# Kernel optimization log

Hardware: AMD Instinct MI355X
Metric: run time of the kernel (lower is better)

## Reference

```python
import jax, jax.numpy as jnp
import numpy as np

N = 50000
E = 800000
IN_DIM = 256
HID = 128
OUT = 64


def setup_inputs() -> dict:
    key = jax.random.key(0)
    ks = jax.random.split(key, 12)
    inp = {}
    inp["x"] = jax.random.normal(ks[0], (N, IN_DIM), dtype=jnp.float32)
    inp["edge_index"] = jax.random.randint(ks[1], (2, E), 0, N, dtype=jnp.int64)
    s0 = 1.0 / np.sqrt(IN_DIM)
    inp["W0"] = jax.random.uniform(ks[2], (IN_DIM, HID), jnp.float32, -s0, s0)
    inp["b0"] = jax.random.uniform(ks[3], (HID,), jnp.float32, -s0, s0)
    sa = 1.0 / np.sqrt(2 * HID)
    inp["att_w1"] = jax.random.uniform(ks[4], (2 * HID, 1), jnp.float32, -sa, sa)
    inp["att_b1"] = jax.random.uniform(ks[5], (1,), jnp.float32, -sa, sa)
    inp["eps1"] = jnp.float32(0.1)
    inp["att_w2"] = jax.random.uniform(ks[6], (2 * HID, 1), jnp.float32, -sa, sa)
    inp["att_b2"] = jax.random.uniform(ks[7], (1,), jnp.float32, -sa, sa)
    inp["eps2"] = jnp.float32(0.1)
    sc = 1.0 / np.sqrt(HID)
    inp["Wc"] = jax.random.uniform(ks[8], (HID, OUT), jnp.float32, -sc, sc)
    inp["bc"] = jax.random.uniform(ks[9], (OUT,), jnp.float32, -sc, sc)
    return inp


def _fagcn_layer(x, row, col, att_w, att_b, eps):
    # x: [N, H]; row/col: [E]
    x_i = x[row]                       # [E, H] source (gathered)
    x_j = x[col]                       # [E, H] destination
    # cat([x_i, x_j]) @ att_w == x_i @ att_w[:H] + x_j @ att_w[H:]
    H = x.shape[1]
    score = x_i @ att_w[:H] + x_j @ att_w[H:] + att_b  # [E, 1]
    alpha = jnp.tanh(score)            # [E, 1]
    messages = alpha * x_i             # [E, H]
    agg = jax.ops.segment_sum(messages, col, num_segments=x.shape[0])  # [N, H]
    return eps * x + (1.0 - eps) * agg


def reference(x, edge_index, W0, b0, att_w1, att_b1, eps1, att_w2, att_b2, eps2, Wc, bc):
    row, col = edge_index[0], edge_index[1]
    h = jax.nn.relu(x @ W0 + b0)       # initial linear + relu (dropout=eval identity)
    h = jax.nn.relu(_fagcn_layer(h, row, col, att_w1, att_b1, eps1))
    h = jax.nn.relu(_fagcn_layer(h, row, col, att_w2, att_b2, eps2))
    return h @ Wc + bc                 # [N, OUT]
```

## Files before the change

### kernel.cpp

```cpp
#include <hip/hip_runtime.h>

#define N_NODES 50000
#define E_EDGES 800000
#define IN_DIM 256
#define HID 128
#define OUT_DIM 64
#define SLOT 64
#define RSLOT 16

#define LR 64
#define KS 64
#define KP 72
#define HP 136

#define NBUILD ((E_EDGES / 8 + 255) / 256)
#define NLIN ((N_NODES + LR - 1) / LR)


typedef unsigned short u16;
typedef __attribute__((ext_vector_type(8))) short short8;
typedef __attribute__((ext_vector_type(4))) float floatx4;

__device__ __forceinline__ u16 f2bf(float f) {
    unsigned u = __float_as_uint(f);
    unsigned r = (u + 0x7FFFu + ((u >> 16) & 1u)) >> 16;
    return (u16)r;
}
__device__ __forceinline__ void bf8_unpack(uint4 v, float* f) {
    f[0] = __uint_as_float(v.x << 16); f[1] = __uint_as_float(v.x & 0xffff0000u);
    f[2] = __uint_as_float(v.y << 16); f[3] = __uint_as_float(v.y & 0xffff0000u);
    f[4] = __uint_as_float(v.z << 16); f[5] = __uint_as_float(v.z & 0xffff0000u);
    f[6] = __uint_as_float(v.w << 16); f[7] = __uint_as_float(v.w & 0xffff0000u);
}
__device__ __forceinline__ uint4 bf8_pack(const float* f) {
    uint4 o;
    o.x = f2bf(f[0]) | ((unsigned)f2bf(f[1]) << 16);
    o.y = f2bf(f[2]) | ((unsigned)f2bf(f[3]) << 16);
    o.z = f2bf(f[4]) | ((unsigned)f2bf(f[5]) << 16);
    o.w = f2bf(f[6]) | ((unsigned)f2bf(f[7]) << 16);
    return o;
}

__global__ __launch_bounds__(256) void k_pre(const float* __restrict__ W0,
                                             const float* __restrict__ Wc,
                                             u16* __restrict__ W0T,
                                             u16* __restrict__ Wct,
                                             int* __restrict__ cnt8) {
    const int gid = blockIdx.x * 256 + threadIdx.x;
    for (int i = gid; i < 8 * N_NODES / 4; i += 32768)
        ((int4*)cnt8)[i] = (int4){0, 0, 0, 0};
    if (gid < IN_DIM * HID) {
        const int n = gid >> 8, k = gid & (IN_DIM - 1);
        W0T[gid] = f2bf(W0[k * HID + n]);
    }
    if (gid < HID * OUT_DIM) {
        const int o = gid >> 7, k = gid & (HID - 1);
        Wct[gid] = f2bf(Wc[k * OUT_DIM + o]);
    }
}

__global__ __launch_bounds__(256) void k_front(
    const float* __restrict__ x, const u16* __restrict__ W0T,
    const float* __restrict__ b0, const float* __restrict__ aw1,
    u16* __restrict__ h, float* __restrict__ sa, float* __restrict__ sb,
    const int* __restrict__ ei, int* __restrict__ cnt8,
    u16* __restrict__ srcidx2) {
    __shared__ u16 As[LR][KP];
    __shared__ u16 Bs[HID][KP];

    if (blockIdx.x < NBUILD) {
        int xcd;
        asm volatile("s_getreg_b32 %0, hwreg(HW_REG_XCC_ID, 0, 32)" : "=s"(xcd));
        xcd &= 7;
        const int cbase = xcd * N_NODES;
        const int rbase = xcd * (N_NODES * RSLOT);
        const int gid = blockIdx.x * 256 + threadIdx.x;
        if (gid >= E_EDGES / 8) return;
        const int4 w0 = ((const int4*)ei)[2 * gid];
        const int4 w1 = ((const int4*)ei)[2 * gid + 1];
        const int4 c0 = ((const int4*)(ei + E_EDGES))[2 * gid];
        const int4 c1 = ((const int4*)(ei + E_EDGES))[2 * gid + 1];
        #define AADD(c) __hip_atomic_fetch_add(&cnt8[cbase + (c)], 1, \
                        __ATOMIC_RELAXED, __HIP_MEMORY_SCOPE_WORKGROUP)
        const int p0 = AADD(c0.x);
        const int p1 = AADD(c0.y);
        const int p2 = AADD(c0.z);
        const int p3 = AADD(c0.w);
        const int p4 = AADD(c1.x);
        const int p5 = AADD(c1.y);
        const int p6 = AADD(c1.z);
        const int p7 = AADD(c1.w);
        #undef AADD
        if (p0 < RSLOT) srcidx2[rbase + (c0.x << 4) + p0] = (u16)w0.x;
        if (p1 < RSLOT) srcidx2[rbase + (c0.y << 4) + p1] = (u16)w0.y;
        if (p2 < RSLOT) srcidx2[rbase + (c0.z << 4) + p2] = (u16)w0.z;
        if (p3 < RSLOT) srcidx2[rbase + (c0.w << 4) + p3] = (u16)w0.w;
        if (p4 < RSLOT) srcidx2[rbase + (c1.x << 4) + p4] = (u16)w1.x;
        if (p5 < RSLOT) srcidx2[rbase + (c1.y << 4) + p5] = (u16)w1.y;
        if (p6 < RSLOT) srcidx2[rbase + (c1.z << 4) + p6] = (u16)w1.z;
        if (p7 < RSLOT) srcidx2[rbase + (c1.w << 4) + p7] = (u16)w1.w;
        return;
    }

    const int t = threadIdx.x;
    const int lane = t & 63;
    const int w = t >> 6;
    const int sub = lane & 15;
    const int quad = lane >> 4;
    const int row0 = (blockIdx.x - NBUILD) * LR;

    floatx4 acc[8];
    #pragma unroll
    for (int i = 0; i < 8; ++i) acc[i] = (floatx4){0.f, 0.f, 0.f, 0.f};

    const int ar = t >> 2;
    const int ak = (t & 3) * 16;
    const int sr = t >> 1;
    const int sk = (t & 1) * 32;

    for (int k0 = 0; k0 < IN_DIM; k0 += KS) {
        {
            int gr = row0 + ar;
            if (gr > N_NODES - 1) gr = N_NODES - 1;
            const float* src = x + (size_t)gr * IN_DIM + k0 + ak;
            #pragma unroll
            for (int i = 0; i < 2; ++i) {
                float4 f0 = ((const float4*)src)[2 * i];
                float4 f1 = ((const float4*)src)[2 * i + 1];
                uint4 p;
                p.x = f2bf(f0.x) | ((unsigned)f2bf(f0.y) << 16);
                p.y = f2bf(f0.z) | ((unsigned)f2bf(f0.w) << 16);
                p.z = f2bf(f1.x) | ((unsigned)f2bf(f1.y) << 16);
                p.w = f2bf(f1.z) | ((unsigned)f2bf(f1.w) << 16);
                *(uint4*)&As[ar][ak + 8 * i] = p;
            }
            const u16* wsrc = W0T + (size_t)sr * IN_DIM + k0 + sk;
            #pragma unroll
            for (int i = 0; i < 4; ++i)
                *(uint4*)&Bs[sr][sk + 8 * i] = ((const uint4*)wsrc)[i];
        }
        __syncthreads();
        #pragma unroll
        for (int kk = 0; kk < KS; kk += 32) {
            short8 a0 = *(const short8*)&As[w * 16 + sub][kk + quad * 8];
            #pragma unroll
            for (int ct = 0; ct < 8; ++ct) {
                short8 bb = *(const short8*)&Bs[ct * 16 + sub][kk + quad * 8];
                acc[ct] = __builtin_amdgcn_mfma_f32_16x16x32_bf16(a0, bb, acc[ct], 0, 0, 0);
            }
        }
        __syncthreads();
    }

    float bias[8], w1c[8], w2c[8];
    #pragma unroll
    for (int ct = 0; ct < 8; ++ct) {
        const int col = ct * 16 + sub;
        bias[ct] = b0[col];
        w1c[ct] = aw1[col];
        w2c[ct] = aw1[HID + col];
    }
    #pragma unroll
    for (int reg = 0; reg < 4; ++reg) {
        const int gr = row0 + w * 16 + quad * 4 + reg;
        const bool ok = gr < N_NODES;
        float ps = 0.f, pd = 0.f;
        #pragma unroll
        for (int ct = 0; ct < 8; ++ct) {
            const float val = fmaxf(acc[ct][reg] + bias[ct], 0.f);
            if (ok) h[(size_t)gr * HID + ct * 16 + sub] = f2bf(val);
            ps += val * w1c[ct];
            pd += val * w2c[ct];
        }
        #pragma unroll
        for (int off = 1; off < 16; off <<= 1) {
            ps += __shfl_xor(ps, off);
            pd += __shfl_xor(pd, off);
        }
        if (sub == 0 && ok) { sa[gr] = ps; sb[gr] = pd; }
    }
}

template <bool REG>
__global__ __launch_bounds__(256) void k_agg(const u16* __restrict__ hin,
                                             const float* __restrict__ sa,
                                             const float* __restrict__ sb,
                                             const float* __restrict__ attb,
                                             const float* __restrict__ epsp,
                                             const int* __restrict__ cnt_or_deg,
                                             const u16* __restrict__ srcin,
                                             u16* __restrict__ hout,
                                             const float* __restrict__ attw_next,
                                             float* __restrict__ sa_next,
                                             float* __restrict__ sb_next,
                                             u16* __restrict__ srcout,
                                             int* __restrict__ degout) {
    __shared__ u16 elist[REG ? 16 : 1][SLOT];
    const int qid = threadIdx.x >> 4;
    const int sub = threadIdx.x & 15;
    const int n = blockIdx.x * 16 + qid;
    if (n >= N_NODES) return;
    const float b = attb[0];
    const float sbn = sb[n];

    int deg;
    if constexpr (REG) {
        int c = 0;
        if (sub < 8) {
            c = cnt_or_deg[sub * N_NODES + n];
            if (c > RSLOT) c = RSLOT;
        }
        int scan = c;
        #pragma unroll
        for (int d = 1; d < 8; d <<= 1) {
            const int tv = __shfl_up(scan, d, 16);
            if (sub >= d) scan += tv;
        }
        const int off = scan - c;
        int D = __shfl(scan, 7, 16);
        if (D > SLOT) D = SLOT;
        if (sub < 8 && c > 0) {
            const u16* s2 = srcin + (size_t)sub * (N_NODES * RSLOT) + ((size_t)n << 4);
            const uint4 i0 = *(const uint4*)s2;
            const uint4 i1 = *(const uint4*)(s2 + 8);
            const unsigned dw[8] = {i0.x, i0.y, i0.z, i0.w, i1.x, i1.y, i1.z, i1.w};
            #pragma unroll
            for (int j = 0; j < 16; ++j) {
                const u16 val = (u16)(dw[j >> 1] >> ((j & 1) * 16));
                const int dp = off + j;
                if (j < c && dp < SLOT) elist[qid][dp] = val;
            }
        }
        deg = D;
        if (sub < 8 && sub * 8 < deg)
            *(uint4*)(srcout + ((size_t)n << 6) + sub * 8) =
                *(const uint4*)&elist[qid][sub * 8];
        if (sub == 0) degout[n] = deg;
    } else {
        deg = cnt_or_deg[n];
        if (deg > SLOT) deg = SLOT;
    }

    float acc[8];
    #pragma unroll
    for (int j = 0; j < 8; ++j) acc[j] = 0.f;

    const u16* dlist = REG ? nullptr : srcin + ((size_t)n << 6);
    int le = 0;
    uint4 svn;
    if constexpr (!REG) { if (le + 8 <= deg) svn = *(const uint4*)(dlist); }
    for (; le + 8 <= deg; le += 8) {
        uint4 sv;
        if constexpr (REG) {
            sv = *(const uint4*)&elist[qid][le];
        } else {
            sv = svn;
            if (le + 16 <= deg) svn = *(const uint4*)(dlist + le + 8);
        }
        int s[8];
        s[0] = (int)(sv.x & 0xffffu); s[1] = (int)(sv.x >> 16);
        s[2] = (int)(sv.y & 0xffffu); s[3] = (int)(sv.y >> 16);
        s[4] = (int)(sv.z & 0xffffu); s[5] = (int)(sv.z >> 16);
        s[6] = (int)(sv.w & 0xffffu); s[7] = (int)(sv.w >> 16);
        uint4 v[8];
        #pragma unroll
        for (int i = 0; i < 8; ++i)
            v[i] = *(const uint4*)(hin + (size_t)s[i] * HID + sub * 8);
        const float tt = tanhf(sa[s[sub & 7]] + sbn + b);
        float al[8];
        #pragma unroll
        for (int i = 0; i < 8; ++i) al[i] = __shfl(tt, i, 16);
        #pragma unroll
        for (int i = 0; i < 8; ++i) {
            float f[8];
            bf8_unpack(v[i], f);
            #pragma unroll
            for (int j = 0; j < 8; ++j) acc[j] += al[i] * f[j];
        }
    }
    const int rem = deg - le;
    if (rem > 0) {
        int s[8];
        if constexpr (REG) {
            const uint4 sv = *(const uint4*)&elist[qid][le];
            int sr8[8];
            sr8[0] = (int)(sv.x & 0xffffu); sr8[1] = (int)(sv.x >> 16);
            sr8[2] = (int)(sv.y & 0xffffu); sr8[3] = (int)(sv.y >> 16);
            sr8[4] = (int)(sv.z & 0xffffu); sr8[5] = (int)(sv.z >> 16);
            sr8[6] = (int)(sv.w & 0xffffu); sr8[7] = (int)(sv.w >> 16);
            #pragma unroll
            for (int i = 0; i < 8; ++i) s[i] = (i < rem) ? sr8[i] : sr8[0];
        } else {
            const int sfirst = (int)dlist[le];
            #pragma unroll
            for (int i = 0; i < 8; ++i) s[i] = (i < rem) ? (int)dlist[le + i] : sfirst;
        }
        const float tt = ((sub & 7) < rem) ? tanhf(sa[s[sub & 7]] + sbn + b) : 0.f;
        float al[8];
        #pragma unroll
        for (int i = 0; i < 8; ++i) al[i] = __shfl(tt, i, 16);
        #pragma unroll
        for (int i = 0; i < 8; ++i) {
            if (i < rem) {
                const uint4 v = *(const uint4*)(hin + (size_t)s[i] * HID + sub * 8);
                float f[8];
                bf8_unpack(v, f);
                #pragma unroll
                for (int j = 0; j < 8; ++j) acc[j] += al[i] * f[j];
            }
        }
    }

    const float eps = epsp[0];
    const float om = 1.f - eps;
    const uint4 sv = *(const uint4*)(hin + (size_t)n * HID + sub * 8);
    float self[8], hv[8];
    bf8_unpack(sv, self);
    #pragma unroll
    for (int j = 0; j < 8; ++j)
        hv[j] = fmaxf(eps * self[j] + om * acc[j], 0.f);
    *(uint4*)(hout + (size_t)n * HID + sub * 8) = bf8_pack(hv);

    if (attw_next != nullptr) {
        float psum = 0.f, dsum = 0.f;
        #pragma unroll
        for (int j = 0; j < 8; ++j) {
            psum += hv[j] * attw_next[sub * 8 + j];
            dsum += hv[j] * attw_next[HID + sub * 8 + j];
        }
        #pragma unroll
        for (int off = 1; off < 16; off <<= 1) {
            psum += __shfl_xor(psum, off);
            dsum += __shfl_xor(dsum, off);
        }
        if (sub == 0) { sa_next[n] = psum; sb_next[n] = dsum; }
    }
}

__global__ __launch_bounds__(256) void k_out_mfma(const u16* __restrict__ h,
                                                  const u16* __restrict__ Wct,
                                                  const float* __restrict__ bc,
                                                  float* __restrict__ out) {
    __shared__ u16 Hs[LR][HP];
    const int t = threadIdx.x;
    const int lane = t & 63;
    const int w = t >> 6;
    const int sub = lane & 15;
    const int quad = lane >> 4;
    const int row0 = blockIdx.x * LR;

    {
        const int hr = t >> 2;
        const int hc = (t & 3) * 32;
        int gr = row0 + hr;
        if (gr > N_NODES - 1) gr = N_NODES - 1;
        const u16* src = h + (size_t)gr * HID + hc;
        #pragma unroll
        for (int i = 0; i < 4; ++i)
            *(uint4*)&Hs[hr][hc + 8 * i] = ((const uint4*)src)[i];
    }
    __syncthreads();

    floatx4 acc[4];
    #pragma unroll
    for (int j = 0; j < 4; ++j) acc[j] = (floatx4){0.f, 0.f, 0.f, 0.f};

    #pragma unroll
    for (int ks = 0; ks < 4; ++ks) {
        const int ko = ks * 32 + quad * 8;
        short8 a = *(const short8*)&Hs[w * 16 + sub][ko];
        #pragma unroll
        for (int ct = 0; ct < 4; ++ct) {
            short8 bb = *(const short8*)(Wct + (ct * 16 + sub) * HID + ko);
            acc[ct] = __builtin_amdgcn_mfma_f32_16x16x32_bf16(a, bb, acc[ct], 0, 0, 0);
        }
    }

    #pragma unroll
    for (int ct = 0; ct < 4; ++ct) {
        const float bias = bc[ct * 16 + sub];
        #pragma unroll
        for (int reg = 0; reg < 4; ++reg) {
            const int gr = row0 + w * 16 + quad * 4 + reg;
            if (gr < N_NODES)
                out[(size_t)gr * OUT_DIM + ct * 16 + sub] = acc[ct][reg] + bias;
        }
    }
}

extern "C" void kernel_launch(void* const* d_in, const int* in_sizes, int n_in,
                              void* d_out, int out_size, void* d_ws, size_t ws_size,
                              hipStream_t stream) {
    const float* x   = (const float*)d_in[0];
    const int*   ei  = (const int*)d_in[1];
    const float* W0  = (const float*)d_in[2];
    const float* b0  = (const float*)d_in[3];
    const float* aw1 = (const float*)d_in[4];
    const float* ab1 = (const float*)d_in[5];
    const float* e1  = (const float*)d_in[6];
    const float* aw2 = (const float*)d_in[7];
    const float* ab2 = (const float*)d_in[8];
    const float* e2  = (const float*)d_in[9];
    const float* Wc  = (const float*)d_in[10];
    const float* bc  = (const float*)d_in[11];
    float* out = (float*)d_out;

    u16* hA  = (u16*)d_ws;
    u16* hB  = hA + (size_t)N_NODES * HID;
    u16* W0T = hB + (size_t)N_NODES * HID;
    u16* Wct = W0T + IN_DIM * HID;
    float* sa1 = (float*)(Wct + HID * OUT_DIM);
    float* sb1 = sa1 + N_NODES;
    float* sa2 = sb1 + N_NODES;
    float* sb2 = sa2 + N_NODES;
    int* deg    = (int*)(sb2 + N_NODES);
    u16* srcidx = (u16*)(deg + N_NODES);
    int* cnt8   = (int*)(srcidx + (size_t)N_NODES * SLOT);
    u16* srcidx2 = (u16*)d_out;

    k_pre<<<128, 256, 0, stream>>>(W0, Wc, W0T, Wct, cnt8);
    k_front<<<NBUILD + NLIN, 256, 0, stream>>>(x, W0T, b0, aw1, hA, sa1, sb1,
                                               ei, cnt8, srcidx2);
    k_agg<true><<<(N_NODES + 15) / 16, 256, 0, stream>>>(
        hA, sa1, sb1, ab1, e1, cnt8, srcidx2, hB, aw2, sa2, sb2, srcidx, deg);
    k_agg<false><<<(N_NODES + 15) / 16, 256, 0, stream>>>(
        hB, sa2, sb2, ab2, e2, deg, srcidx, hA, nullptr, nullptr, nullptr,
        nullptr, nullptr);
    k_out_mfma<<<NLIN, 256, 0, stream>>>(hA, Wct, bc, out);
}
```

Before: 234.0 us.

## Prefetch full x row slice into registers and batch more edges per build thread

The linear front path now loads all four K-slices of the thread's x row into registers up front and converts them to bf16 before the MFMA loop. This takes global-load latency out of the per-slice sync loop, at the cost of much higher register pressure. The edge-bucketing path now gives each thread 16 edges, up from 8, which cuts the number of build blocks. That raises per-thread atomic work but lowers launch and scheduling overhead.

```diff
diff --git a/kernel.cpp b/kernel.cpp
--- a/kernel.cpp
+++ b/kernel.cpp
@@ -13,7 +13,8 @@
 #define KP 72
 #define HP 136
 
-#define NBUILD ((E_EDGES / 8 + 255) / 256)
+#define EPT 16
+#define NBUILD ((E_EDGES + 256 * EPT - 1) / (256 * EPT))
 #define NLIN ((N_NODES + LR - 1) / LR)
 
 
@@ -73,32 +74,27 @@
         asm volatile("s_getreg_b32 %0, hwreg(HW_REG_XCC_ID, 0, 32)" : "=s"(xcd));
         xcd &= 7;
         const int cbase = xcd * N_NODES;
-        const int rbase = xcd * (N_NODES * RSLOT);
-        const int gid = blockIdx.x * 256 + threadIdx.x;
-        if (gid >= E_EDGES / 8) return;
-        const int4 w0 = ((const int4*)ei)[2 * gid];
-        const int4 w1 = ((const int4*)ei)[2 * gid + 1];
-        const int4 c0 = ((const int4*)(ei + E_EDGES))[2 * gid];
-        const int4 c1 = ((const int4*)(ei + E_EDGES))[2 * gid + 1];
-        #define AADD(c) __hip_atomic_fetch_add(&cnt8[cbase + (c)], 1, \
-                        __ATOMIC_RELAXED, __HIP_MEMORY_SCOPE_WORKGROUP)
-        const int p0 = AADD(c0.x);
-        const int p1 = AADD(c0.y);
-        const int p2 = AADD(c0.z);
-        const int p3 = AADD(c0.w);
-        const int p4 = AADD(c1.x);
-        const int p5 = AADD(c1.y);
-        const int p6 = AADD(c1.z);
-        const int p7 = AADD(c1.w);
-        #undef AADD
-        if (p0 < RSLOT) srcidx2[rbase + (c0.x << 4) + p0] = (u16)w0.x;
-        if (p1 < RSLOT) srcidx2[rbase + (c0.y << 4) + p1] = (u16)w0.y;
-        if (p2 < RSLOT) srcidx2[rbase + (c0.z << 4) + p2] = (u16)w0.z;
-        if (p3 < RSLOT) srcidx2[rbase + (c0.w << 4) + p3] = (u16)w0.w;
-        if (p4 < RSLOT) srcidx2[rbase + (c1.x << 4) + p4] = (u16)w1.x;
-        if (p5 < RSLOT) srcidx2[rbase + (c1.y << 4) + p5] = (u16)w1.y;
-        if (p6 < RSLOT) srcidx2[rbase + (c1.z << 4) + p6] = (u16)w1.z;
-        if (p7 < RSLOT) srcidx2[rbase + (c1.w << 4) + p7] = (u16)w1.w;
+        const int rb = xcd * (N_NODES * RSLOT);
+        const int base = (blockIdx.x * 256 + threadIdx.x) * EPT;
+        #pragma unroll
+        for (int g = 0; g < EPT / 4; ++g) {
+            const int eb = base + g * 4;
+            if (eb < E_EDGES) {
+                const int4 w = ((const int4*)ei)[eb >> 2];
+                const int4 c = ((const int4*)(ei + E_EDGES))[eb >> 2];
+                #define AADD(cc) __hip_atomic_fetch_add(&cnt8[cbase + (cc)], 1, \
+                                __ATOMIC_RELAXED, __HIP_MEMORY_SCOPE_WORKGROUP)
+                const int q0 = AADD(c.x);
+                const int q1 = AADD(c.y);
+                const int q2 = AADD(c.z);
+                const int q3 = AADD(c.w);
+                #undef AADD
+                if (q0 < RSLOT) srcidx2[rb + (c.x << 4) + q0] = (u16)w.x;
+                if (q1 < RSLOT) srcidx2[rb + (c.y << 4) + q1] = (u16)w.y;
+                if (q2 < RSLOT) srcidx2[rb + (c.z << 4) + q2] = (u16)w.z;
+                if (q3 < RSLOT) srcidx2[rb + (c.w << 4) + q3] = (u16)w.w;
+            }
+        }
         return;
     }
 
@@ -109,36 +105,48 @@
     const int quad = lane >> 4;
     const int row0 = (blockIdx.x - NBUILD) * LR;
 
-    floatx4 acc[8];
-    #pragma unroll
-    for (int i = 0; i < 8; ++i) acc[i] = (floatx4){0.f, 0.f, 0.f, 0.f};
-
     const int ar = t >> 2;
     const int ak = (t & 3) * 16;
     const int sr = t >> 1;
     const int sk = (t & 1) * 32;
 
-    for (int k0 = 0; k0 < IN_DIM; k0 += KS) {
-        {
-            int gr = row0 + ar;
-            if (gr > N_NODES - 1) gr = N_NODES - 1;
-            const float* src = x + (size_t)gr * IN_DIM + k0 + ak;
-            #pragma unroll
-            for (int i = 0; i < 2; ++i) {
-                float4 f0 = ((const float4*)src)[2 * i];
-                float4 f1 = ((const float4*)src)[2 * i + 1];
-                uint4 p;
-                p.x = f2bf(f0.x) | ((unsigned)f2bf(f0.y) << 16);
-                p.y = f2bf(f0.z) | ((unsigned)f2bf(f0.w) << 16);
-                p.z = f2bf(f1.x) | ((unsigned)f2bf(f1.y) << 16);
-                p.w = f2bf(f1.z) | ((unsigned)f2bf(f1.w) << 16);
-                *(uint4*)&As[ar][ak + 8 * i] = p;
-            }
-            const u16* wsrc = W0T + (size_t)sr * IN_DIM + k0 + sk;
-            #pragma unroll
-            for (int i = 0; i < 4; ++i)
-                *(uint4*)&Bs[sr][sk + 8 * i] = ((const uint4*)wsrc)[i];
-        }
+    int gr_a = row0 + ar;
+    if (gr_a > N_NODES - 1) gr_a = N_NODES - 1;
+    const float* xsrc = x + (size_t)gr_a * IN_DIM + ak;
+    float4 xr[4][4];
+    #pragma unroll
+    for (int s = 0; s < 4; ++s)
+        #pragma unroll
+        for (int i = 0; i < 4; ++i)
+            xr[s][i] = ((const float4*)(xsrc + s * KS))[i];
+    uint4 xa[4][2];
+    #pragma unroll
+    for (int s = 0; s < 4; ++s)
+        #pragma unroll
+        for (int i = 0; i < 2; ++i) {
+            const float4 f0 = xr[s][2 * i];
+            const float4 f1 = xr[s][2 * i + 1];
+            uint4 pk;
+            pk.x = f2bf(f0.x) | ((unsigned)f2bf(f0.y) << 16);
+            pk.y = f2bf(f0.z) | ((unsigned)f2bf(f0.w) << 16);
+            pk.z = f2bf(f1.x) | ((unsigned)f2bf(f1.y) << 16);
+            pk.w = f2bf(f1.z) | ((unsigned)f2bf(f1.w) << 16);
+            xa[s][i] = pk;
+        }
+
+    floatx4 acc[8];
+    #pragma unroll
+    for (int i = 0; i < 8; ++i) acc[i] = (floatx4){0.f, 0.f, 0.f, 0.f};
+
+    #pragma unroll
+    for (int s = 0; s < 4; ++s) {
+        const int k0 = s * KS;
+        *(uint4*)&As[ar][ak] = xa[s][0];
+        *(uint4*)&As[ar][ak + 8] = xa[s][1];
+        const u16* wsrc = W0T + (size_t)sr * IN_DIM + k0 + sk;
+        #pragma unroll
+        for (int i = 0; i < 4; ++i)
+            *(uint4*)&Bs[sr][sk + 8 * i] = ((const uint4*)wsrc)[i];
         __syncthreads();
         #pragma unroll
         for (int kk = 0; kk < KS; kk += 32) {
```

Measured after the change: 244.1 us. 1.04x slower.
